# Kernel tuning notes

Hardware: AMD Instinct MI355X
Metric: run time of the kernel (lower is better)

The kernel has to match this reference:

```python
import jax, jax.numpy as jnp
import numpy as np

NFEAT = 256; NHID = 256; NHEADS = 4; DH = NHID // NHEADS; ALPHA = 0.2
B, T, N = 16, 6, 128
NTOT = B * T * N
DEG = 16
E = NTOT * DEG


def setup_inputs() -> dict:
    key = jax.random.key(0)
    ks = jax.random.split(key, 12)
    s = 0.05
    emb = jax.random.normal(ks[0], (B, T, N, NFEAT), jnp.float32)
    nmask = jnp.ones((B, T, N), jnp.float32)
    nodeidx = jnp.arange(NTOT, dtype=jnp.int32)
    # batched-DGL-style edges: random intra-graph edges, avg in-degree DEG
    rng = np.random.default_rng(0)
    TN = T * N
    goff = (np.arange(E) // (TN * DEG)) * TN  # graph block offset per edge
    edge_src = jnp.asarray(rng.integers(0, TN, E) + goff, jnp.int32)
    edge_dst = jnp.asarray(rng.integers(0, TN, E) + goff, jnp.int32)
    tid = jnp.asarray((np.arange(NTOT) // N) % T, jnp.int32)  # turn id per node
    W = jax.random.normal(ks[1], (NFEAT, NHID), jnp.float32) * s
    a_src = jax.random.normal(ks[2], (NHEADS, DH), jnp.float32) * s
    a_dst = jax.random.normal(ks[3], (NHEADS, DH), jnp.float32) * s
    Wz = jax.random.normal(ks[4], (NHID, NHID), jnp.float32) * s
    Uz = jax.random.normal(ks[5], (NHID, NHID), jnp.float32) * s
    Wr = jax.random.normal(ks[6], (NHID, NHID), jnp.float32) * s
    Ur = jax.random.normal(ks[7], (NHID, NHID), jnp.float32) * s
    Wn = jax.random.normal(ks[8], (NHID, NHID), jnp.float32) * s
    Un = jax.random.normal(ks[9], (NHID, NHID), jnp.float32) * s
    bz = jnp.zeros((NHID,), jnp.float32)
    br = jnp.zeros((NHID,), jnp.float32)
    bn = jnp.zeros((NHID,), jnp.float32)
    return dict(emb=emb, nmask=nmask, W=W, a_src=a_src, a_dst=a_dst,
                Wz=Wz, Uz=Uz, Wr=Wr, Ur=Ur, Wn=Wn, Un=Un, bz=bz, br=br, bn=bn,
                nodeidx=nodeidx, edge_src=edge_src, edge_dst=edge_dst, tid=tid)


def reference(emb, nmask, W, a_src, a_dst, Wz, Uz, Wr, Ur, Wn, Un, bz, br, bn,
              nodeidx, edge_src, edge_dst, tid):
    seg_sum = jax.ops.segment_sum
    # set_node_feature: masked utterance embeddings gathered into node order
    feat = (emb * nmask[..., None]).reshape(NTOT, NFEAT)[nodeidx]
    h = feat
    e_attn = None
    # propagation: 6 turn-wise GATGRU updates
    for t in range(T):
        Wh = (h @ W).reshape(NTOT, NHEADS, DH)            # [Ntot,H,Dh]
        es = jnp.sum(Wh * a_src, axis=-1)                 # [Ntot,H]
        ed = jnp.sum(Wh * a_dst, axis=-1)
        logit = jax.nn.leaky_relu(es[edge_src] + ed[edge_dst], ALPHA)  # [E,H]
        # segment softmax over incoming edges of each dst node
        mx = jax.ops.segment_max(logit, edge_dst, num_segments=NTOT)
        mx = jnp.where(jnp.isfinite(mx), mx, 0.0)
        w = jnp.exp(logit - mx[edge_dst])
        den = seg_sum(w, edge_dst, num_segments=NTOT)
        attn = w / (den[edge_dst] + 1e-9)                 # [E,H]
        msg = seg_sum(attn[..., None] * Wh[edge_src], edge_dst,
                      num_segments=NTOT).reshape(NTOT, NHID)
        # GRU update, applied only to nodes of the current turn
        z = jax.nn.sigmoid(msg @ Wz + h @ Uz + bz)
        r = jax.nn.sigmoid(msg @ Wr + h @ Ur + br)
        n = jnp.tanh(msg @ Wn + (r * h) @ Un + bn)
        hn = (1.0 - z) * h + z * n
        h = jnp.where((tid == t)[:, None], hn, h)
        e_attn = attn
    # pooling: attn_score[v] = sum of edge attention into v (copy_e + sum)
    attn_score = seg_sum(e_attn.mean(axis=-1), edge_dst, num_segments=NTOT)
    # read_out_loud: per-graph per-turn softmax-weighted mean, split even/odd turns
    a = jax.nn.softmax(attn_score.reshape(B, T, N), axis=-1)  # softmax within turn
    pooled = jnp.mean(h.reshape(B, T, N, NHID) * a[..., None], axis=2)  # [B,T,nhid]
    r1 = pooled[:, 0::2].sum(axis=1)[:, None, :]  # speaker 1: even turns, [B,1,nhid]
    r2 = pooled[:, 1::2].sum(axis=1)[:, None, :]  # speaker 2: odd turns
    return r1, r2
```

## Files before the change

### kernel.cpp

```cpp
#include <hip/hip_runtime.h>

#define NTOT 12288
#define NE   196608
#define MAXDEG 64

typedef __attribute__((ext_vector_type(8))) short bf8_t;
typedef __attribute__((ext_vector_type(4))) float f32x4;

__device__ __forceinline__ int turn_row_map(int r, int t) {
  return (r >> 7) * 768 + t * 128 + (r & 127);
}

__device__ __forceinline__ void splitbf(float x, unsigned short& hi, unsigned short& lo) {
  unsigned u = __float_as_uint(x);
  hi = (unsigned short)(u >> 16);
  float fh = __uint_as_float(u & 0xFFFF0000u);
  lo = (unsigned short)(__float_as_uint(x - fh) >> 16);
}
__device__ __forceinline__ float reconf(unsigned short hi, unsigned short lo) {
  return __uint_as_float((unsigned)hi << 16) + __uint_as_float((unsigned)lo << 16);
}
__device__ __forceinline__ uint2 pack4(unsigned short a, unsigned short b,
                                       unsigned short c, unsigned short d) {
  return make_uint2((unsigned)a | ((unsigned)b << 16), (unsigned)c | ((unsigned)d << 16));
}

__global__ void __launch_bounds__(256)
k_prep(const float* __restrict__ emb, const float* __restrict__ nmask,
       const int* __restrict__ nodeidx,
       const float* __restrict__ W, const float* __restrict__ Wz,
       const float* __restrict__ Wr, const float* __restrict__ Wn,
       const float* __restrict__ Uz, const float* __restrict__ Ur,
       const float* __restrict__ Un,
       const int* __restrict__ esrc, const int* __restrict__ edst, int* __restrict__ cnt,
       unsigned short* __restrict__ hbh, unsigned short* __restrict__ hbl,
       unsigned short* __restrict__ wth, unsigned short* __restrict__ wtl,
       unsigned short* __restrict__ adj) {
  int l = blockIdx.x, tid = threadIdx.x;
  if (l < 3072) {
    int i = l * 256 + tid;
    int row = i >> 6;
    int src = nodeidx[row];
    float m = nmask[src];
    float4 v = ((const float4*)emb)[(size_t)src * 64 + (i & 63)];
    v.x *= m; v.y *= m; v.z *= m; v.w *= m;
    unsigned short h0,l0,h1,l1,h2,l2,h3,l3;
    splitbf(v.x,h0,l0); splitbf(v.y,h1,l1); splitbf(v.z,h2,l2); splitbf(v.w,h3,l3);
    int o = row * 256 + (i & 63) * 4;
    *(uint2*)(hbh + o) = pack4(h0,h1,h2,h3);
    *(uint2*)(hbl + o) = pack4(l0,l1,l2,l3);
  } else if (l < 3184) {
    __shared__ float ldt[64][65];
    int bidx = l - 3072;
    int g = bidx >> 4, ti = bidx & 15;
    int tk = (ti & 3) * 64, tn = (ti >> 2) * 64;
    const float* M = g==0?W : g==1?Wz : g==2?Wr : g==3?Wn : g==4?Uz : g==5?Ur : Un;
#pragma unroll
    for (int p = 0; p < 16; p++) {
      int r = p * 4 + (tid >> 6);
      ldt[r][tid & 63] = M[(size_t)(tk + r) * 256 + tn + (tid & 63)];
    }
    __syncthreads();
#pragma unroll
    for (int p = 0; p < 16; p++) {
      int nl_ = p * 4 + (tid >> 6);
      int kl = tid & 63;
      float v = ldt[kl][nl_];
      unsigned short hh, ll; splitbf(v, hh, ll);
      int idx = (g * 256 + tn + nl_) * 256 + tk + kl;
      wth[idx] = hh; wtl[idx] = ll;
    }
  } else {
    int e = (l - 3184) * 256 + tid;
    int d = edst[e];
    int pos = atomicAdd(&cnt[d], 1);
    if (pos < MAXDEG) adj[(size_t)d * MAXDEG + pos] = (unsigned short)esrc[e];
  }
}

template <int MODE>
__global__ void __launch_bounds__(256)
k_mf(const unsigned short* __restrict__ aph, const unsigned short* __restrict__ apl,
     const unsigned short* __restrict__ wth, const unsigned short* __restrict__ wtl,
     float* __restrict__ Wh,
     unsigned short* __restrict__ hbh, unsigned short* __restrict__ hbl,
     float* __restrict__ g1, float* __restrict__ uacc,
     unsigned short* __restrict__ rbh, unsigned short* __restrict__ rbl,
     const float* __restrict__ bz, const float* __restrict__ br,
     const float* __restrict__ bn,
     const float* __restrict__ asrc, const float* __restrict__ adst,
     float* __restrict__ es, float* __restrict__ ed, float* __restrict__ outp, int t) {
  __shared__ __align__(16) unsigned short Ah[32][72], Al[32][72];
  __shared__ __align__(16) unsigned short Bh[64][72], Bl[64][72];
  __shared__ float esb[32][2], edb[32][2];
  int l = blockIdx.x;
  int tid = threadIdx.x;
  if constexpr (MODE == 3) {
    if (l >= 256) {
      ((float4*)outp)[(l - 256) * 256 + tid] = make_float4(0.f, 0.f, 0.f, 0.f);
      return;
    }
  }
  int q = 0;
  int bx, by;
  if constexpr (MODE == 5) {
    q = (l < 1536) ? 0 : (l < 3072 ? 1 : 2);
    if (q == 0) { bx = (l & 31) >> 3; by = (l >> 5) * 8 + (l & 7); }
    else { int l2 = l - (q == 1 ? 1536 : 3072); bx = (l2 & 63) >> 3; by = (l2 >> 6) * 8 + (l2 & 7); }
  } else if constexpr (MODE == 2) { bx = (l % 96) >> 3; by = (l / 96) * 8 + (l & 7); }
  else                            { bx = (l & 31) >> 3; by = (l >> 5) * 8 + (l & 7); }

  int ar = tid >> 3, aq = tid & 7;
  int bn_ = tid >> 2, bq = tid & 3;
  int gmA = by * 32 + ar;
  int arow;
  if constexpr (MODE == 1) arow = turn_row_map(gmA, t);
  else if constexpr (MODE == 5) {
    if (q == 0) arow = gmA;
    else arow = (gmA / 384) * 768 + (((q == 2) ? 3 : 0) + ((gmA % 384) >> 7)) * 128 + (gmA & 127);
  } else arow = gmA;
  const unsigned short* ahp = aph + (size_t)arow * 256;
  const unsigned short* alp = apl + (size_t)arow * 256;

  int nbase;
  if constexpr (MODE == 5)      nbase = (q == 0) ? bx * 64 : 1024 + bx * 64;
  else if constexpr (MODE == 1) nbase = bx * 64;
  else if constexpr (MODE == 2) nbase = 256 + bx * 64;
  else                          nbase = 1536 + bx * 64;
  const unsigned short* bhp = wth + (size_t)(nbase + bn_) * 256;
  const unsigned short* blp = wtl + (size_t)(nbase + bn_) * 256;

  int lane = tid & 63, wv = tid >> 6;
  int rh = wv >> 1, ch = wv & 1;
  int quad = lane >> 4, nl = lane & 15;
  f32x4 acc0 = {0.f, 0.f, 0.f, 0.f}, acc1 = {0.f, 0.f, 0.f, 0.f};

  for (int k0 = 0; k0 < 256; k0 += 64) {
    *(uint4*)&Ah[ar][aq * 8] = *(const uint4*)(ahp + k0 + aq * 8);
    *(uint4*)&Al[ar][aq * 8] = *(const uint4*)(alp + k0 + aq * 8);
    *(uint4*)&Bh[bn_][bq * 16]     = *(const uint4*)(bhp + k0 + bq * 16);
    *(uint4*)&Bh[bn_][bq * 16 + 8] = *(const uint4*)(bhp + k0 + bq * 16 + 8);
    *(uint4*)&Bl[bn_][bq * 16]     = *(const uint4*)(blp + k0 + bq * 16);
    *(uint4*)&Bl[bn_][bq * 16 + 8] = *(const uint4*)(blp + k0 + bq * 16 + 8);
    __syncthreads();
#pragma unroll
    for (int kk = 0; kk < 64; kk += 32) {
      bf8_t a_h = *(const bf8_t*)&Ah[rh * 16 + nl][kk + quad * 8];
      bf8_t a_l = *(const bf8_t*)&Al[rh * 16 + nl][kk + quad * 8];
      bf8_t bh0 = *(const bf8_t*)&Bh[ch * 32 + nl][kk + quad * 8];
      bf8_t bl0 = *(const bf8_t*)&Bl[ch * 32 + nl][kk + quad * 8];
      bf8_t bh1 = *(const bf8_t*)&Bh[ch * 32 + 16 + nl][kk + quad * 8];
      bf8_t bl1 = *(const bf8_t*)&Bl[ch * 32 + 16 + nl][kk + quad * 8];
      acc0 = __builtin_amdgcn_mfma_f32_16x16x32_bf16(a_h, bh0, acc0, 0, 0, 0);
      acc1 = __builtin_amdgcn_mfma_f32_16x16x32_bf16(a_h, bh1, acc1, 0, 0, 0);
      acc0 = __builtin_amdgcn_mfma_f32_16x16x32_bf16(a_h, bl0, acc0, 0, 0, 0);
      acc1 = __builtin_amdgcn_mfma_f32_16x16x32_bf16(a_h, bl1, acc1, 0, 0, 0);
      acc0 = __builtin_amdgcn_mfma_f32_16x16x32_bf16(a_l, bh0, acc0, 0, 0, 0);
      acc1 = __builtin_amdgcn_mfma_f32_16x16x32_bf16(a_l, bh1, acc1, 0, 0, 0);
    }
    __syncthreads();
  }

  int gr = by * 32 + rh * 16 + quad * 4;
  if constexpr (MODE == 5 || MODE == 1) {
    if (MODE == 5 && q != 0) {
      int rbase = (q == 2) ? 6144 : 0;
#pragma unroll
      for (int r = 0; r < 4; r++) {
        int grr = gr + r;
#pragma unroll
        for (int ct = 0; ct < 2; ct++) {
          float D = (ct == 0) ? acc0[r] : acc1[r];
          int col = bx * 64 + ch * 32 + ct * 16 + nl;
          float bias = (col < 256) ? bz[col] : br[col - 256];
          uacc[(size_t)(rbase + grr) * 512 + col] = D + bias;
        }
      }
    } else {
      int c0 = bx * 64 + ch * 32 + nl, c1 = c0 + 16;
      float a0 = asrc[c0], a1 = asrc[c1], d0 = adst[c0], d1 = adst[c1];
      float pes[4], ped[4];
#pragma unroll
      for (int r = 0; r < 4; r++) {
        int v = (MODE == 5) ? (gr + r) : turn_row_map(gr + r, t);
        float x0 = acc0[r], x1 = acc1[r];
        Wh[(size_t)v * 256 + c0] = x0;
        Wh[(size_t)v * 256 + c1] = x1;
        pes[r] = x0 * a0 + x1 * a1;
        ped[r] = x0 * d0 + x1 * d1;
      }
#pragma unroll
      for (int m = 1; m < 16; m <<= 1)
#pragma unroll
        for (int r = 0; r < 4; r++) {
          pes[r] += __shfl_xor(pes[r], m);
          ped[r] += __shfl_xor(ped[r], m);
        }
      if (nl == 0)
#pragma unroll
        for (int r = 0; r < 4; r++) {
          esb[rh * 16 + quad * 4 + r][ch] = pes[r];
          edb[rh * 16 + quad * 4 + r][ch] = ped[r];
        }
      __syncthreads();
      if (tid < 32) {
        int m = tid;
        int v = (MODE == 5) ? (by * 32 + m) : turn_row_map(by * 32 + m, t);
        es[v * 4 + bx] = esb[m][0] + esb[m][1];
        ed[v * 4 + bx] = edb[m][0] + edb[m][1];
      }
    }
  } else if constexpr (MODE == 2) {
    int g = bx >> 2;
    int tm3 = t % 3;
    const float* up = uacc + (size_t)(t >= 3 ? 6144 : 0) * 512;
#pragma unroll
    for (int r = 0; r < 4; r++) {
      int grr = gr + r;
      int v = turn_row_map(grr, t);
      int urow = (grr >> 7) * 384 + tm3 * 128 + (grr & 127);
#pragma unroll
      for (int ct = 0; ct < 2; ct++) {
        float D = (ct == 0) ? acc0[r] : acc1[r];
        int c = (bx & 3) * 64 + ch * 32 + ct * 16 + nl;
        if (g == 0) {
          g1[(size_t)grr * 512 + c] = D + up[(size_t)urow * 512 + c];
        } else if (g == 1) {
          float rpre = D + up[(size_t)urow * 512 + 256 + c];
          float rv = 1.f / (1.f + __expf(-rpre));
          int hidx = v * 256 + c;
          float hv = reconf(hbh[hidx], hbl[hidx]);
          float rhv = rv * hv;
          unsigned short hh, ll; splitbf(rhv, hh, ll);
          rbh[grr * 256 + c] = hh; rbl[grr * 256 + c] = ll;
        } else {
          g1[(size_t)grr * 512 + 256 + c] = D + bn[c];
        }
      }
    }
  } else {
#pragma unroll
    for (int r = 0; r < 4; r++) {
      int grr = gr + r;
      int v = turn_row_map(grr, t);
#pragma unroll
      for (int ct = 0; ct < 2; ct++) {
        float D = (ct == 0) ? acc0[r] : acc1[r];
        int c = bx * 64 + ch * 32 + ct * 16 + nl;
        float zpre = g1[(size_t)grr * 512 + c];
        float npre = g1[(size_t)grr * 512 + 256 + c] + D;
        float z = 1.f / (1.f + __expf(-zpre));
        float n = tanhf(npre);
        int hidx = v * 256 + c;
        float hv = reconf(hbh[hidx], hbl[hidx]);
        float hn = (1.f - z) * hv + z * n;
        unsigned short hh, ll; splitbf(hn, hh, ll);
        hbh[hidx] = hh;
        hbl[hidx] = ll;
      }
    }
  }
}

__global__ void __launch_bounds__(256)
k_attn(const int* __restrict__ cnt, const unsigned short* __restrict__ adj,
       const float* __restrict__ es, const float* __restrict__ ed,
       const float* __restrict__ Wh,
       unsigned short* __restrict__ mbh, unsigned short* __restrict__ mbl,
       float* __restrict__ score, int t, int allnodes) {
  __shared__ float wgs[4][64][4];
  __shared__ unsigned short ssrc[4][64];
  int gph = blockIdx.x & 15, j = blockIdx.x >> 4;
  int wv = threadIdx.x >> 6;
  int w = (allnodes ? gph * 768 : gph * 128) + j * 4 + wv;
  int lane = threadIdx.x & 63;
  int v, mrow, storemsg;
  if (allnodes) {
    v = w;
    int bt = v >> 7;
    int tt = bt % 6;
    storemsg = (tt == t);
    mrow = (bt / 6) * 128 + (v & 127);
  } else {
    v = turn_row_map(w, t);
    mrow = w;
    storemsg = 1;
  }
  int deg = cnt[v];
  if (deg > MAXDEG) deg = MAXDEG;
  const unsigned short* row = adj + (size_t)v * MAXDEG;
  float edq = ed[v * 4 + (lane & 3)];
  float dsum = 0.f;
  int passes = (deg + 15) >> 4;
  for (int p = 0; p < passes; p++) {
    int jj = p * 16 + (lane >> 2);
    if (jj < deg) {
      int s = row[jj];
      float lg = es[s * 4 + (lane & 3)] + edq;
      lg = lg >= 0.f ? lg : 0.2f * lg;
      float wgv = __expf(lg);
      wgs[wv][jj][lane & 3] = wgv;
      if ((lane & 3) == 0) ssrc[wv][jj] = (unsigned short)s;
      dsum += wgv;
    } else {
      wgs[wv][jj][lane & 3] = 0.f;
      if ((lane & 3) == 0) ssrc[wv][jj] = 0;
    }
  }
  dsum += __shfl_xor(dsum, 4);
  dsum += __shfl_xor(dsum, 8);
  dsum += __shfl_xor(dsum, 16);
  dsum += __shfl_xor(dsum, 32);
  float invq = 1.f / (dsum + 1e-9f);
  if (allnodes) {
    float val = dsum * invq;
    val += __shfl_xor(val, 1);
    val += __shfl_xor(val, 2);
    if (lane == 0) score[v] = 0.25f * val;
  }
  if (storemsg) {
    float myinv = __shfl(invq, lane >> 4);
    float4 acc = make_float4(0.f, 0.f, 0.f, 0.f);
    int deg4 = (deg + 3) & ~3;
    for (int j0 = 0; j0 < deg4; j0 += 4) {
#pragma unroll
      for (int u = 0; u < 4; u++) {
        int s = ssrc[wv][j0 + u];
        float wgv = wgs[wv][j0 + u][lane >> 4];
        float4 x = ((const float4*)Wh)[(size_t)s * 64 + lane];
        acc.x += wgv * x.x; acc.y += wgv * x.y;
        acc.z += wgv * x.z; acc.w += wgv * x.w;
      }
    }
    unsigned short h0,l0,h1,l1,h2,l2,h3,l3;
    splitbf(acc.x * myinv, h0, l0); splitbf(acc.y * myinv, h1, l1);
    splitbf(acc.z * myinv, h2, l2); splitbf(acc.w * myinv, h3, l3);
    int o = mrow * 256 + lane * 4;
    *(uint2*)(mbh + o) = pack4(h0, h1, h2, h3);
    *(uint2*)(mbl + o) = pack4(l0, l1, l2, l3);
  }
}

__global__ void __launch_bounds__(256)
k_pool(const float* __restrict__ score,
       const unsigned short* __restrict__ hbh,
       const unsigned short* __restrict__ hbl,
       float* __restrict__ out) {
  __shared__ float a[128];
  __shared__ float red[8];
  int bt = blockIdx.x;
  int base = bt * 128;
  int tid = threadIdx.x;
  float v = (tid < 128) ? score[base + tid] : -1e30f;
  float m = v;
#pragma unroll
  for (int s = 1; s < 64; s <<= 1) m = fmaxf(m, __shfl_xor(m, s));
  if ((tid & 63) == 0) red[tid >> 6] = m;
  __syncthreads();
  float mx = fmaxf(red[0], red[1]);
  float e = (tid < 128) ? __expf(v - mx) : 0.f;
  if (tid < 128) a[tid] = e;
  float s_ = e;
#pragma unroll
  for (int s = 1; s < 64; s <<= 1) s_ += __shfl_xor(s_, s);
  if ((tid & 63) == 0) red[4 + (tid >> 6)] = s_;
  __syncthreads();
  float sinv = 1.f / ((red[4] + red[5]) * 128.f);
  float acc = 0.f;
  for (int n = 0; n < 128; n++) {
    int idx = (base + n) * 256 + tid;
    acc += a[n] * reconf(hbh[idx], hbl[idx]);
  }
  int b = bt / 6, tt = bt % 6, spk = tt & 1;
  atomicAdd(&out[spk * 4096 + b * 256 + tid], acc * sinv);
}

extern "C" void kernel_launch(void* const* d_in, const int* in_sizes, int n_in,
                              void* d_out, int out_size, void* d_ws, size_t ws_size,
                              hipStream_t stream) {
  const float* emb    = (const float*)d_in[0];
  const float* nmask  = (const float*)d_in[1];
  const float* W      = (const float*)d_in[2];
  const float* a_src  = (const float*)d_in[3];
  const float* a_dst  = (const float*)d_in[4];
  const float* Wz     = (const float*)d_in[5];
  const float* Uz     = (const float*)d_in[6];
  const float* Wr     = (const float*)d_in[7];
  const float* Ur     = (const float*)d_in[8];
  const float* Wn     = (const float*)d_in[9];
  const float* Un     = (const float*)d_in[10];
  const float* bz     = (const float*)d_in[11];
  const float* br     = (const float*)d_in[12];
  const float* bn     = (const float*)d_in[13];
  const int* nodeidx  = (const int*)d_in[14];
  const int* esrc     = (const int*)d_in[15];
  const int* edst     = (const int*)d_in[16];
  float* out = (float*)d_out;

  char* ws = (char*)d_ws;
  size_t off = 0;
  auto carve = [&](size_t bytes) { char* p = ws + off; off += (bytes + 255) & ~(size_t)255; return p; };
  float* Wh     = (float*)carve(NTOT * 256 * 4);
  unsigned short* hbh = (unsigned short*)carve(NTOT * 256 * 2);
  unsigned short* hbl = (unsigned short*)carve(NTOT * 256 * 2);
  unsigned short* mbh = (unsigned short*)carve(2048 * 256 * 2);
  unsigned short* mbl = (unsigned short*)carve(2048 * 256 * 2);
  unsigned short* rbh = (unsigned short*)carve(2048 * 256 * 2);
  unsigned short* rbl = (unsigned short*)carve(2048 * 256 * 2);
  float* es     = (float*)carve(NTOT * 4 * 4);
  float* ed     = (float*)carve(NTOT * 4 * 4);
  float* g1     = (float*)carve(2048 * 512 * 4);
  float* uacc   = (float*)carve((size_t)12288 * 512 * 4);
  float* score  = (float*)carve(NTOT * 4);
  int*   cnt    = (int*)carve(NTOT * 4);
  unsigned short* adj = (unsigned short*)carve((size_t)NTOT * MAXDEG * 2);
  unsigned short* wth = (unsigned short*)carve(1792 * 256 * 2);
  unsigned short* wtl = (unsigned short*)carve(1792 * 256 * 2);
  if (off > ws_size) return;

  hipMemsetAsync(cnt, 0, NTOT * 4, stream);
  k_prep<<<3952, 256, 0, stream>>>(emb, nmask, nodeidx, W, Wz, Wr, Wn, Uz, Ur, Un,
                                   esrc, edst, cnt, hbh, hbl, wth, wtl, adj);
  k_mf<5><<<4608, 256, 0, stream>>>(hbh, hbl, wth, wtl, Wh, hbh, hbl, g1, uacc,
                                    rbh, rbl, bz, br, bn, a_src, a_dst, es, ed, out, 0);

  for (int t = 0; t < 6; t++) {
    if (t > 0) {
      k_mf<1><<<256, 256, 0, stream>>>(hbh, hbl, wth, wtl, Wh, hbh, hbl, g1, uacc,
                                       rbh, rbl, bz, br, bn, a_src, a_dst, es, ed, out, t - 1);
    }
    if (t < 5)
      k_attn<<<512, 256, 0, stream>>>(cnt, adj, es, ed, Wh, mbh, mbl, score, t, 0);
    else
      k_attn<<<3072, 256, 0, stream>>>(cnt, adj, es, ed, Wh, mbh, mbl, score, t, 1);
    k_mf<2><<<768, 256, 0, stream>>>(mbh, mbl, wth, wtl, Wh, hbh, hbl, g1, uacc,
                                     rbh, rbl, bz, br, bn, a_src, a_dst, es, ed, out, t);
    k_mf<3><<<(t == 5 ? 264 : 256), 256, 0, stream>>>(rbh, rbl, wth, wtl, Wh, hbh, hbl,
                                                      g1, uacc, rbh, rbl, bz, br, bn,
                                                      a_src, a_dst, es, ed, out, t);
  }

  k_pool<<<96, 256, 0, stream>>>(score, hbh, hbl, out);
}
```

Before: 312.6 us.

## Fuse per-turn attention aggregation and GRU GEMMs into one kernel per turn

Replaces the per-turn attention, GRU-gate and candidate GEMM kernels with one fused kernel. Each block computes the messages for 16 nodes into shared memory, runs the z/r/n GEMMs directly from L2-resident weights, and writes the updated hidden state. The kernel that recomputes Wh for the updated turn now uses the same 16-row tile form, and the attention score used for pooling is recomputed inside the pool kernel. This removes several launches per turn and the global round-trips for messages, r*h and gate pre-activations. In exchange the per-turn grid drops to 128 blocks, which leaves much of the GPU idle, and the weights are read from global memory instead of shared tiles.

```diff
diff --git a/kernel.cpp b/kernel.cpp
--- a/kernel.cpp
+++ b/kernel.cpp
@@ -1,7 +1,6 @@
 #include <hip/hip_runtime.h>
 
 #define NTOT 12288
-#define NE   196608
 #define MAXDEG 64
 
 typedef __attribute__((ext_vector_type(8))) short bf8_t;
@@ -23,6 +22,31 @@
 __device__ __forceinline__ uint2 pack4(unsigned short a, unsigned short b,
                                        unsigned short c, unsigned short d) {
   return make_uint2((unsigned)a | ((unsigned)b << 16), (unsigned)c | ((unsigned)d << 16));
+}
+
+template <int NB>
+__device__ __forceinline__ void gemm16(const unsigned short (&AH)[16][264],
+                                       const unsigned short (&AL)[16][264],
+                                       const unsigned short* __restrict__ wth,
+                                       const unsigned short* __restrict__ wtl,
+                                       int wv, int quad, int nl, f32x4 (&acc)[4]) {
+  const f32x4 vz = {0.f, 0.f, 0.f, 0.f};
+#pragma unroll
+  for (int ct = 0; ct < 4; ct++) acc[ct] = vz;
+#pragma unroll
+  for (int kk = 0; kk < 256; kk += 32) {
+    bf8_t a_h = *(const bf8_t*)&AH[nl][kk + quad * 8];
+    bf8_t a_l = *(const bf8_t*)&AL[nl][kk + quad * 8];
+#pragma unroll
+    for (int ct = 0; ct < 4; ct++) {
+      size_t bo = (size_t)(NB + wv * 64 + ct * 16 + nl) * 256 + kk + quad * 8;
+      bf8_t bh = *(const bf8_t*)(wth + bo);
+      bf8_t bl = *(const bf8_t*)(wtl + bo);
+      acc[ct] = __builtin_amdgcn_mfma_f32_16x16x32_bf16(a_h, bh, acc[ct], 0, 0, 0);
+      acc[ct] = __builtin_amdgcn_mfma_f32_16x16x32_bf16(a_h, bl, acc[ct], 0, 0, 0);
+      acc[ct] = __builtin_amdgcn_mfma_f32_16x16x32_bf16(a_l, bh, acc[ct], 0, 0, 0);
+    }
+  }
 }
 
 __global__ void __launch_bounds__(256)
@@ -78,55 +102,31 @@
   }
 }
 
-template <int MODE>
 __global__ void __launch_bounds__(256)
-k_mf(const unsigned short* __restrict__ aph, const unsigned short* __restrict__ apl,
-     const unsigned short* __restrict__ wth, const unsigned short* __restrict__ wtl,
-     float* __restrict__ Wh,
-     unsigned short* __restrict__ hbh, unsigned short* __restrict__ hbl,
-     float* __restrict__ g1, float* __restrict__ uacc,
-     unsigned short* __restrict__ rbh, unsigned short* __restrict__ rbl,
-     const float* __restrict__ bz, const float* __restrict__ br,
-     const float* __restrict__ bn,
-     const float* __restrict__ asrc, const float* __restrict__ adst,
-     float* __restrict__ es, float* __restrict__ ed, float* __restrict__ outp, int t) {
+k_mf5(const unsigned short* __restrict__ aph, const unsigned short* __restrict__ apl,
+      const unsigned short* __restrict__ wth, const unsigned short* __restrict__ wtl,
+      float* __restrict__ Wh, float* __restrict__ uacc,
+      const float* __restrict__ bz, const float* __restrict__ br,
+      const float* __restrict__ asrc, const float* __restrict__ adst,
+      float* __restrict__ es, float* __restrict__ ed) {
   __shared__ __align__(16) unsigned short Ah[32][72], Al[32][72];
   __shared__ __align__(16) unsigned short Bh[64][72], Bl[64][72];
   __shared__ float esb[32][2], edb[32][2];
-  int l = blockIdx.x;
-  int tid = threadIdx.x;
-  if constexpr (MODE == 3) {
-    if (l >= 256) {
-      ((float4*)outp)[(l - 256) * 256 + tid] = make_float4(0.f, 0.f, 0.f, 0.f);
-      return;
-    }
-  }
-  int q = 0;
+  int l = blockIdx.x, tid = threadIdx.x;
+  int q = (l < 1536) ? 0 : (l < 3072 ? 1 : 2);
   int bx, by;
-  if constexpr (MODE == 5) {
-    q = (l < 1536) ? 0 : (l < 3072 ? 1 : 2);
-    if (q == 0) { bx = (l & 31) >> 3; by = (l >> 5) * 8 + (l & 7); }
-    else { int l2 = l - (q == 1 ? 1536 : 3072); bx = (l2 & 63) >> 3; by = (l2 >> 6) * 8 + (l2 & 7); }
-  } else if constexpr (MODE == 2) { bx = (l % 96) >> 3; by = (l / 96) * 8 + (l & 7); }
-  else                            { bx = (l & 31) >> 3; by = (l >> 5) * 8 + (l & 7); }
+  if (q == 0) { bx = (l & 31) >> 3; by = (l >> 5) * 8 + (l & 7); }
+  else { int l2 = l - (q == 1 ? 1536 : 3072); bx = (l2 & 63) >> 3; by = (l2 >> 6) * 8 + (l2 & 7); }
 
   int ar = tid >> 3, aq = tid & 7;
   int bn_ = tid >> 2, bq = tid & 3;
   int gmA = by * 32 + ar;
   int arow;
-  if constexpr (MODE == 1) arow = turn_row_map(gmA, t);
-  else if constexpr (MODE == 5) {
-    if (q == 0) arow = gmA;
-    else arow = (gmA / 384) * 768 + (((q == 2) ? 3 : 0) + ((gmA % 384) >> 7)) * 128 + (gmA & 127);
-  } else arow = gmA;
+  if (q == 0) arow = gmA;
+  else arow = (gmA / 384) * 768 + (((q == 2) ? 3 : 0) + ((gmA % 384) >> 7)) * 128 + (gmA & 127);
   const unsigned short* ahp = aph + (size_t)arow * 256;
   const unsigned short* alp = apl + (size_t)arow * 256;
-
-  int nbase;
-  if constexpr (MODE == 5)      nbase = (q == 0) ? bx * 64 : 1024 + bx * 64;
-  else if constexpr (MODE == 1) nbase = bx * 64;
-  else if constexpr (MODE == 2) nbase = 256 + bx * 64;
-  else                          nbase = 1536 + bx * 64;
+  int nbase = (q == 0) ? bx * 64 : 1024 + bx * 64;
   const unsigned short* bhp = wth + (size_t)(nbase + bn_) * 256;
   const unsigned short* blp = wtl + (size_t)(nbase + bn_) * 256;
 
@@ -162,163 +162,157 @@
   }
 
   int gr = by * 32 + rh * 16 + quad * 4;
-  if constexpr (MODE == 5 || MODE == 1) {
-    if (MODE == 5 && q != 0) {
-      int rbase = (q == 2) ? 6144 : 0;
-#pragma unroll
-      for (int r = 0; r < 4; r++) {
-        int grr = gr + r;
-#pragma unroll
-        for (int ct = 0; ct < 2; ct++) {
-          float D = (ct == 0) ? acc0[r] : acc1[r];
-          int col = bx * 64 + ch * 32 + ct * 16 + nl;
-          float bias = (col < 256) ? bz[col] : br[col - 256];
-          uacc[(size_t)(rbase + grr) * 512 + col] = D + bias;
-        }
-      }
-    } else {
-      int c0 = bx * 64 + ch * 32 + nl, c1 = c0 + 16;
-      float a0 = asrc[c0], a1 = asrc[c1], d0 = adst[c0], d1 = adst[c1];
-      float pes[4], ped[4];
-#pragma unroll
-      for (int r = 0; r < 4; r++) {
-        int v = (MODE == 5) ? (gr + r) : turn_row_map(gr + r, t);
-        float x0 = acc0[r], x1 = acc1[r];
-        Wh[(size_t)v * 256 + c0] = x0;
-        Wh[(size_t)v * 256 + c1] = x1;
-        pes[r] = x0 * a0 + x1 * a1;
-        ped[r] = x0 * d0 + x1 * d1;
-      }
-#pragma unroll
-      for (int m = 1; m < 16; m <<= 1)
-#pragma unroll
-        for (int r = 0; r < 4; r++) {
-          pes[r] += __shfl_xor(pes[r], m);
-          ped[r] += __shfl_xor(ped[r], m);
-        }
-      if (nl == 0)
-#pragma unroll
-        for (int r = 0; r < 4; r++) {
-          esb[rh * 16 + quad * 4 + r][ch] = pes[r];
-          edb[rh * 16 + quad * 4 + r][ch] = ped[r];
-        }
-      __syncthreads();
-      if (tid < 32) {
-        int m = tid;
-        int v = (MODE == 5) ? (by * 32 + m) : turn_row_map(by * 32 + m, t);
-        es[v * 4 + bx] = esb[m][0] + esb[m][1];
-        ed[v * 4 + bx] = edb[m][0] + edb[m][1];
-      }
-    }
-  } else if constexpr (MODE == 2) {
-    int g = bx >> 2;
-    int tm3 = t % 3;
-    const float* up = uacc + (size_t)(t >= 3 ? 6144 : 0) * 512;
+  if (q != 0) {
+    int rbase = (q == 2) ? 6144 : 0;
 #pragma unroll
     for (int r = 0; r < 4; r++) {
       int grr = gr + r;
-      int v = turn_row_map(grr, t);
-      int urow = (grr >> 7) * 384 + tm3 * 128 + (grr & 127);
 #pragma unroll
       for (int ct = 0; ct < 2; ct++) {
         float D = (ct == 0) ? acc0[r] : acc1[r];
-        int c = (bx & 3) * 64 + ch * 32 + ct * 16 + nl;
-        if (g == 0) {
-          g1[(size_t)grr * 512 + c] = D + up[(size_t)urow * 512 + c];
-        } else if (g == 1) {
-          float rpre = D + up[(size_t)urow * 512 + 256 + c];
-          float rv = 1.f / (1.f + __expf(-rpre));
-          int hidx = v * 256 + c;
-          float hv = reconf(hbh[hidx], hbl[hidx]);
-          float rhv = rv * hv;
-          unsigned short hh, ll; splitbf(rhv, hh, ll);
-          rbh[grr * 256 + c] = hh; rbl[grr * 256 + c] = ll;
-        } else {
-          g1[(size_t)grr * 512 + 256 + c] = D + bn[c];
-        }
+        int col = bx * 64 + ch * 32 + ct * 16 + nl;
+        float bias = (col < 256) ? bz[col] : br[col - 256];
+        uacc[(size_t)(rbase + grr) * 512 + col] = D + bias;
       }
     }
   } else {
-#pragma unroll
-    for (int r = 0; r < 4; r++) {
-      int grr = gr + r;
-      int v = turn_row_map(grr, t);
-#pragma unroll
-      for (int ct = 0; ct < 2; ct++) {
-        float D = (ct == 0) ? acc0[r] : acc1[r];
-        int c = bx * 64 + ch * 32 + ct * 16 + nl;
-        float zpre = g1[(size_t)grr * 512 + c];
-        float npre = g1[(size_t)grr * 512 + 256 + c] + D;
-        float z = 1.f / (1.f + __expf(-zpre));
-        float n = tanhf(npre);
-        int hidx = v * 256 + c;
-        float hv = reconf(hbh[hidx], hbl[hidx]);
-        float hn = (1.f - z) * hv + z * n;
-        unsigned short hh, ll; splitbf(hn, hh, ll);
-        hbh[hidx] = hh;
-        hbl[hidx] = ll;
-      }
+    int c0 = bx * 64 + ch * 32 + nl, c1 = c0 + 16;
+    float a0 = asrc[c0], a1 = asrc[c1], d0 = adst[c0], d1 = adst[c1];
+    float pes[4], ped[4];
+#pragma unroll
+    for (int r = 0; r < 4; r++) {
+      int v = gr + r;
+      float x0 = acc0[r], x1 = acc1[r];
+      Wh[(size_t)v * 256 + c0] = x0;
+      Wh[(size_t)v * 256 + c1] = x1;
+      pes[r] = x0 * a0 + x1 * a1;
+      ped[r] = x0 * d0 + x1 * d1;
+    }
+#pragma unroll
+    for (int m = 1; m < 16; m <<= 1)
+#pragma unroll
+      for (int r = 0; r < 4; r++) {
+        pes[r] += __shfl_xor(pes[r], m);
+        ped[r] += __shfl_xor(ped[r], m);
+      }
+    if (nl == 0)
+#pragma unroll
+      for (int r = 0; r < 4; r++) {
+        esb[rh * 16 + quad * 4 + r][ch] = pes[r];
+        edb[rh * 16 + quad * 4 + r][ch] = ped[r];
+      }
+    __syncthreads();
+    if (tid < 32) {
+      int m = tid;
+      int v = by * 32 + m;
+      es[v * 4 + bx] = esb[m][0] + esb[m][1];
+      ed[v * 4 + bx] = edb[m][0] + edb[m][1];
     }
   }
 }
 
 __global__ void __launch_bounds__(256)
-k_attn(const int* __restrict__ cnt, const unsigned short* __restrict__ adj,
-       const float* __restrict__ es, const float* __restrict__ ed,
-       const float* __restrict__ Wh,
-       unsigned short* __restrict__ mbh, unsigned short* __restrict__ mbl,
-       float* __restrict__ score, int t, int allnodes) {
+k_upd(const unsigned short* __restrict__ hbh, const unsigned short* __restrict__ hbl,
+      const unsigned short* __restrict__ wth, const unsigned short* __restrict__ wtl,
+      float* __restrict__ Wh, const float* __restrict__ asrc, const float* __restrict__ adst,
+      float* __restrict__ es, float* __restrict__ ed, int tu) {
+  __shared__ __align__(16) unsigned short Ah[16][264], Al[16][264];
+  int tid = threadIdx.x;
+  int r0 = blockIdx.x * 16;
+  {
+    int row = tid >> 4, cc = (tid & 15) * 16;
+    int v = turn_row_map(r0 + row, tu);
+    const unsigned short* sh = hbh + (size_t)v * 256 + cc;
+    const unsigned short* sl = hbl + (size_t)v * 256 + cc;
+    *(uint4*)&Ah[row][cc]     = *(const uint4*)sh;
+    *(uint4*)&Ah[row][cc + 8] = *(const uint4*)(sh + 8);
+    *(uint4*)&Al[row][cc]     = *(const uint4*)sl;
+    *(uint4*)&Al[row][cc + 8] = *(const uint4*)(sl + 8);
+  }
+  __syncthreads();
+  int lane = tid & 63, wv = tid >> 6;
+  int quad = lane >> 4, nl = lane & 15;
+  f32x4 acc[4];
+  gemm16<0>(Ah, Al, wth, wtl, wv, quad, nl, acc);
+
+  float pes[4] = {0.f, 0.f, 0.f, 0.f}, ped[4] = {0.f, 0.f, 0.f, 0.f};
+#pragma unroll
+  for (int ct = 0; ct < 4; ct++) {
+    int c = wv * 64 + ct * 16 + nl;
+    float ac = asrc[c], dc = adst[c];
+#pragma unroll
+    for (int r = 0; r < 4; r++) {
+      int v = turn_row_map(r0 + quad * 4 + r, tu);
+      float D = acc[ct][r];
+      Wh[(size_t)v * 256 + c] = D;
+      pes[r] += D * ac;
+      ped[r] += D * dc;
+    }
+  }
+#pragma unroll
+  for (int m = 1; m < 16; m <<= 1)
+#pragma unroll
+    for (int r = 0; r < 4; r++) {
+      pes[r] += __shfl_xor(pes[r], m);
+      ped[r] += __shfl_xor(ped[r], m);
+    }
+  if (nl == 0)
+#pragma unroll
+    for (int r = 0; r < 4; r++) {
+      int v = turn_row_map(r0 + quad * 4 + r, tu);
+      es[v * 4 + wv] = pes[r];
+      ed[v * 4 + wv] = ped[r];
+    }
+}
+
+__global__ void __launch_bounds__(256)
+k_atg(const int* __restrict__ cnt, const unsigned short* __restrict__ adj,
+      const float* __restrict__ es, const float* __restrict__ ed,
+      const float* __restrict__ Wh,
+      const unsigned short* __restrict__ wth, const unsigned short* __restrict__ wtl,
+      const float* __restrict__ uacc, const float* __restrict__ bn,
+      unsigned short* __restrict__ hbh, unsigned short* __restrict__ hbl,
+      float* __restrict__ outp, int t) {
+  __shared__ __align__(16) unsigned short mAh[16][264], mAl[16][264];
+  __shared__ __align__(16) unsigned short rAh[16][264], rAl[16][264];
   __shared__ float wgs[4][64][4];
   __shared__ unsigned short ssrc[4][64];
-  int gph = blockIdx.x & 15, j = blockIdx.x >> 4;
-  int wv = threadIdx.x >> 6;
-  int w = (allnodes ? gph * 768 : gph * 128) + j * 4 + wv;
-  int lane = threadIdx.x & 63;
-  int v, mrow, storemsg;
-  if (allnodes) {
-    v = w;
-    int bt = v >> 7;
-    int tt = bt % 6;
-    storemsg = (tt == t);
-    mrow = (bt / 6) * 128 + (v & 127);
-  } else {
-    v = turn_row_map(w, t);
-    mrow = w;
-    storemsg = 1;
-  }
-  int deg = cnt[v];
-  if (deg > MAXDEG) deg = MAXDEG;
-  const unsigned short* row = adj + (size_t)v * MAXDEG;
-  float edq = ed[v * 4 + (lane & 3)];
-  float dsum = 0.f;
-  int passes = (deg + 15) >> 4;
-  for (int p = 0; p < passes; p++) {
-    int jj = p * 16 + (lane >> 2);
-    if (jj < deg) {
-      int s = row[jj];
-      float lg = es[s * 4 + (lane & 3)] + edq;
-      lg = lg >= 0.f ? lg : 0.2f * lg;
-      float wgv = __expf(lg);
-      wgs[wv][jj][lane & 3] = wgv;
-      if ((lane & 3) == 0) ssrc[wv][jj] = (unsigned short)s;
-      dsum += wgv;
-    } else {
-      wgs[wv][jj][lane & 3] = 0.f;
-      if ((lane & 3) == 0) ssrc[wv][jj] = 0;
-    }
-  }
-  dsum += __shfl_xor(dsum, 4);
-  dsum += __shfl_xor(dsum, 8);
-  dsum += __shfl_xor(dsum, 16);
-  dsum += __shfl_xor(dsum, 32);
-  float invq = 1.f / (dsum + 1e-9f);
-  if (allnodes) {
-    float val = dsum * invq;
-    val += __shfl_xor(val, 1);
-    val += __shfl_xor(val, 2);
-    if (lane == 0) score[v] = 0.25f * val;
-  }
-  if (storemsg) {
+  int tid = threadIdx.x;
+  if (blockIdx.x >= 128) {
+    ((float4*)outp)[(blockIdx.x - 128) * 256 + tid] = make_float4(0.f, 0.f, 0.f, 0.f);
+    return;
+  }
+  int r0 = blockIdx.x * 16;
+  int lane = tid & 63, wv = tid >> 6;
+
+  for (int i = 0; i < 4; i++) {
+    int j = wv * 4 + i;
+    int v = turn_row_map(r0 + j, t);
+    int deg = cnt[v]; if (deg > MAXDEG) deg = MAXDEG;
+    const unsigned short* row = adj + (size_t)v * MAXDEG;
+    float edq = ed[v * 4 + (lane & 3)];
+    float dsum = 0.f;
+    int passes = (deg + 15) >> 4;
+    for (int p = 0; p < passes; p++) {
+      int jj = p * 16 + (lane >> 2);
+      if (jj < deg) {
+        int s = row[jj];
+        float lg = es[s * 4 + (lane & 3)] + edq;
+        lg = lg >= 0.f ? lg : 0.2f * lg;
+        float wgv = __expf(lg);
+        wgs[wv][jj][lane & 3] = wgv;
+        if ((lane & 3) == 0) ssrc[wv][jj] = (unsigned short)s;
+        dsum += wgv;
+      } else {
+        wgs[wv][jj][lane & 3] = 0.f;
+        if ((lane & 3) == 0) ssrc[wv][jj] = 0;
+      }
+    }
+    dsum += __shfl_xor(dsum, 4);
+    dsum += __shfl_xor(dsum, 8);
+    dsum += __shfl_xor(dsum, 16);
+    dsum += __shfl_xor(dsum, 32);
+    float invq = 1.f / (dsum + 1e-9f);
     float myinv = __shfl(invq, lane >> 4);
     float4 acc = make_float4(0.f, 0.f, 0.f, 0.f);
     int deg4 = (deg + 3) & ~3;
@@ -335,30 +329,113 @@
     unsigned short h0,l0,h1,l1,h2,l2,h3,l3;
     splitbf(acc.x * myinv, h0, l0); splitbf(acc.y * myinv, h1, l1);
     splitbf(acc.z * myinv, h2, l2); splitbf(acc.w * myinv, h3, l3);
-    int o = mrow * 256 + lane * 4;
-    *(uint2*)(mbh + o) = pack4(h0, h1, h2, h3);
-    *(uint2*)(mbl + o) = pack4(l0, l1, l2, l3);
-  }
+    *(uint2*)&mAh[j][lane * 4] = pack4(h0, h1, h2, h3);
+    *(uint2*)&mAl[j][lane * 4] = pack4(l0, l1, l2, l3);
+  }
+  __syncthreads();
+
+  int quad = lane >> 4, nl = lane & 15;
+  int rbase = (t >= 3) ? 6144 : 0;
+  int tm3 = t % 3;
+  f32x4 zacc[4], nacc[4];
+  gemm16<256>(mAh, mAl, wth, wtl, wv, quad, nl, zacc);
+#pragma unroll
+  for (int ct = 0; ct < 4; ct++)
+#pragma unroll
+    for (int r = 0; r < 4; r++) {
+      int grr = r0 + quad * 4 + r;
+      int c = wv * 64 + ct * 16 + nl;
+      int urow = rbase + (grr >> 7) * 384 + tm3 * 128 + (grr & 127);
+      zacc[ct][r] += uacc[(size_t)urow * 512 + c];
+    }
+  gemm16<768>(mAh, mAl, wth, wtl, wv, quad, nl, nacc);
+#pragma unroll
+  for (int ct = 0; ct < 4; ct++)
+#pragma unroll
+    for (int r = 0; r < 4; r++)
+      nacc[ct][r] += bn[wv * 64 + ct * 16 + nl];
+  {
+    f32x4 racc[4];
+    gemm16<512>(mAh, mAl, wth, wtl, wv, quad, nl, racc);
+#pragma unroll
+    for (int ct = 0; ct < 4; ct++)
+#pragma unroll
+      for (int r = 0; r < 4; r++) {
+        int lr = quad * 4 + r, grr = r0 + lr;
+        int c = wv * 64 + ct * 16 + nl;
+        int urow = rbase + (grr >> 7) * 384 + tm3 * 128 + (grr & 127);
+        float rpre = racc[ct][r] + uacc[(size_t)urow * 512 + 256 + c];
+        float rv = 1.f / (1.f + __expf(-rpre));
+        int v = turn_row_map(grr, t);
+        float hv = reconf(hbh[(size_t)v * 256 + c], hbl[(size_t)v * 256 + c]);
+        unsigned short hh, ll; splitbf(rv * hv, hh, ll);
+        rAh[lr][c] = hh; rAl[lr][c] = ll;
+      }
+  }
+  __syncthreads();
+
+  f32x4 du[4];
+  gemm16<1536>(rAh, rAl, wth, wtl, wv, quad, nl, du);
+#pragma unroll
+  for (int ct = 0; ct < 4; ct++)
+#pragma unroll
+    for (int r = 0; r < 4; r++) {
+      int grr = r0 + quad * 4 + r;
+      int c = wv * 64 + ct * 16 + nl;
+      int v = turn_row_map(grr, t);
+      float z = 1.f / (1.f + __expf(-zacc[ct][r]));
+      float n_ = tanhf(nacc[ct][r] + du[ct][r]);
+      float hv = reconf(hbh[(size_t)v * 256 + c], hbl[(size_t)v * 256 + c]);
+      float hn = (1.f - z) * hv + z * n_;
+      unsigned short hh, ll; splitbf(hn, hh, ll);
+      hbh[(size_t)v * 256 + c] = hh;
+      hbl[(size_t)v * 256 + c] = ll;
+    }
 }
 
 __global__ void __launch_bounds__(256)
-k_pool(const float* __restrict__ score,
-       const unsigned short* __restrict__ hbh,
-       const unsigned short* __restrict__ hbl,
+k_pool(const int* __restrict__ cnt, const unsigned short* __restrict__ adj,
+       const float* __restrict__ es, const float* __restrict__ ed,
+       const unsigned short* __restrict__ hbh, const unsigned short* __restrict__ hbl,
        float* __restrict__ out) {
   __shared__ float a[128];
   __shared__ float red[8];
-  int bt = blockIdx.x;
-  int base = bt * 128;
-  int tid = threadIdx.x;
-  float v = (tid < 128) ? score[base + tid] : -1e30f;
-  float m = v;
+  int bt = blockIdx.x, base = bt * 128, tid = threadIdx.x;
+  {
+    int n = tid >> 1, v = base + n;
+    int deg = cnt[v]; if (deg > MAXDEG) deg = MAXDEG;
+    const unsigned short* row = adj + (size_t)v * MAXDEG;
+    float part = 0.f;
+#pragma unroll
+    for (int hh = 0; hh < 2; hh++) {
+      int h = (tid & 1) * 2 + hh;
+      float edv = ed[v * 4 + h];
+      float den = 0.f;
+      for (int j0 = 0; j0 < deg; j0 += 4) {
+#pragma unroll
+        for (int u = 0; u < 4; u++) {
+          if (j0 + u < deg) {
+            int s = row[j0 + u];
+            float lg = es[s * 4 + h] + edv;
+            lg = lg >= 0.f ? lg : 0.2f * lg;
+            den += __expf(lg);
+          }
+        }
+      }
+      part += den / (den + 1e-9f);
+    }
+    part += __shfl_xor(part, 1);
+    if ((tid & 1) == 0) a[n] = 0.25f * part;
+  }
+  __syncthreads();
+  float sv = (tid < 128) ? a[tid] : -1e30f;
+  float m = sv;
 #pragma unroll
   for (int s = 1; s < 64; s <<= 1) m = fmaxf(m, __shfl_xor(m, s));
   if ((tid & 63) == 0) red[tid >> 6] = m;
   __syncthreads();
   float mx = fmaxf(red[0], red[1]);
-  float e = (tid < 128) ? __expf(v - mx) : 0.f;
+  float e = (tid < 128) ? __expf(sv - mx) : 0.f;
   if (tid < 128) a[tid] = e;
   float s_ = e;
 #pragma unroll
@@ -400,18 +477,12 @@
   char* ws = (char*)d_ws;
   size_t off = 0;
   auto carve = [&](size_t bytes) { char* p = ws + off; off += (bytes + 255) & ~(size_t)255; return p; };
-  float* Wh     = (float*)carve(NTOT * 256 * 4);
-  unsigned short* hbh = (unsigned short*)carve(NTOT * 256 * 2);
-  unsigned short* hbl = (unsigned short*)carve(NTOT * 256 * 2);
-  unsigned short* mbh = (unsigned short*)carve(2048 * 256 * 2);
-  unsigned short* mbl = (unsigned short*)carve(2048 * 256 * 2);
-  unsigned short* rbh = (unsigned short*)carve(2048 * 256 * 2);
-  unsigned short* rbl = (unsigned short*)carve(2048 * 256 * 2);
+  float* Wh     = (float*)carve((size_t)NTOT * 256 * 4);
+  unsigned short* hbh = (unsigned short*)carve((size_t)NTOT * 256 * 2);
+  unsigned short* hbl = (unsigned short*)carve((size_t)NTOT * 256 * 2);
   float* es     = (float*)carve(NTOT * 4 * 4);
   float* ed     = (float*)carve(NTOT * 4 * 4);
-  float* g1     = (float*)carve(2048 * 512 * 4);
   float* uacc   = (float*)carve((size_t)12288 * 512 * 4);
-  float* score  = (float*)carve(NTOT * 4);
   int*   cnt    = (int*)carve(NTOT * 4);
   unsigned short* adj = (unsigned short*)carve((size_t)NTOT * MAXDEG * 2);
   unsigned short* wth = (unsigned short*)carve(1792 * 256 * 2);
@@ -421,24 +492,15 @@
   hipMemsetAsync(cnt, 0, NTOT * 4, stream);
   k_prep<<<3952, 256, 0, stream>>>(emb, nmask, nodeidx, W, Wz, Wr, Wn, Uz, Ur, Un,
                                    esrc, edst, cnt, hbh, hbl, wth, wtl, adj);
-  k_mf<5><<<4608, 256, 0, stream>>>(hbh, hbl, wth, wtl, Wh, hbh, hbl, g1, uacc,
-                                    rbh, rbl, bz, br, bn, a_src, a_dst, es, ed, out, 0);
+  k_mf5<<<4608, 256, 0, stream>>>(hbh, hbl, wth, wtl, Wh, uacc, bz, br,
+                                  a_src, a_dst, es, ed);
 
   for (int t = 0; t < 6; t++) {
-    if (t > 0) {
-      k_mf<1><<<256, 256, 0, stream>>>(hbh, hbl, wth, wtl, Wh, hbh, hbl, g1, uacc,
-                                       rbh, rbl, bz, br, bn, a_src, a_dst, es, ed, out, t - 1);
-    }
-    if (t < 5)
-      k_attn<<<512, 256, 0, stream>>>(cnt, adj, es, ed, Wh, mbh, mbl, score, t, 0);
-    else
-      k_attn<<<3072, 256, 0, stream>>>(cnt, adj, es, ed, Wh, mbh, mbl, score, t, 1);
-    k_mf<2><<<768, 256, 0, stream>>>(mbh, mbl, wth, wtl, Wh, hbh, hbl, g1, uacc,
-                                     rbh, rbl, bz, br, bn, a_src, a_dst, es, ed, out, t);
-    k_mf<3><<<(t == 5 ? 264 : 256), 256, 0, stream>>>(rbh, rbl, wth, wtl, Wh, hbh, hbl,
-                                                      g1, uacc, rbh, rbl, bz, br, bn,
-                                                      a_src, a_dst, es, ed, out, t);
-  }
-
-  k_pool<<<96, 256, 0, stream>>>(score, hbh, hbl, out);
-}
+    if (t > 0)
+      k_upd<<<128, 256, 0, stream>>>(hbh, hbl, wth, wtl, Wh, a_src, a_dst, es, ed, t - 1);
+    k_atg<<<(t == 5 ? 136 : 128), 256, 0, stream>>>(cnt, adj, es, ed, Wh, wth, wtl,
+                                                    uacc, bn, hbh, hbl, out, t);
+  }
+
+  k_pool<<<96, 256, 0, stream>>>(cnt, adj, es, ed, hbh, hbl, out);
+}
```

Measured after the change: 501.2 us. 60.3% more time.
